# Optimization experiments

Hardware: AMD Instinct MI355X
Metric: run time of the kernel (lower is better)

The kernel has to match this reference:

```python
import jax, jax.numpy as jnp
import numpy as np

D_MODEL = 1024
NUM_HEADS = 16
HEAD_DIM = D_MODEL // NUM_HEADS
D_FF = 4 * D_MODEL


def setup_inputs() -> dict:
    key = jax.random.key(0)
    ks = jax.random.split(key, 16)
    s = 0.02
    inp = {
        "x": jax.random.normal(ks[0], (2, 2048, D_MODEL), dtype=jnp.float32),
        "w_q": jax.random.normal(ks[1], (D_MODEL, D_MODEL), dtype=jnp.float32) * s,
        "b_q": jnp.zeros((D_MODEL,), jnp.float32),
        "w_k": jax.random.normal(ks[2], (D_MODEL, D_MODEL), dtype=jnp.float32) * s,
        "b_k": jnp.zeros((D_MODEL,), jnp.float32),
        "w_v": jax.random.normal(ks[3], (D_MODEL, D_MODEL), dtype=jnp.float32) * s,
        "b_v": jnp.zeros((D_MODEL,), jnp.float32),
        "w_o": jax.random.normal(ks[4], (D_MODEL, D_MODEL), dtype=jnp.float32) * s,
        "b_o": jnp.zeros((D_MODEL,), jnp.float32),
        "w_ff1": jax.random.normal(ks[5], (D_MODEL, D_FF), dtype=jnp.float32) * s,
        "b_ff1": jnp.zeros((D_FF,), jnp.float32),
        "w_ff2": jax.random.normal(ks[6], (D_FF, D_MODEL), dtype=jnp.float32) * s,
        "b_ff2": jnp.zeros((D_MODEL,), jnp.float32),
        "ln1_g": jnp.ones((D_MODEL,), jnp.float32),
        "ln1_b": jnp.zeros((D_MODEL,), jnp.float32),
        "ln2_g": jnp.ones((D_MODEL,), jnp.float32),
        "ln2_b": jnp.zeros((D_MODEL,), jnp.float32),
    }
    return inp


def layer_norm(x, g, b, eps=1e-5):
    mu = jnp.mean(x, axis=-1, keepdims=True)
    var = jnp.var(x, axis=-1, keepdims=True)
    return (x - mu) * jax.lax.rsqrt(var + eps) * g + b


def encoder_block(x, w_q, b_q, w_k, b_k, w_v, b_v, w_o, b_o,
                  w_ff1, b_ff1, w_ff2, b_ff2, ln1_g, ln1_b, ln2_g, ln2_b):
    B, S, _ = x.shape
    # QKV projections -> [B, H, S, hd]
    def proj(w, b):
        return (x @ w + b).reshape(B, S, NUM_HEADS, HEAD_DIM).transpose(0, 2, 1, 3)
    q, k, v = proj(w_q, b_q), proj(w_k, b_k), proj(w_v, b_v)
    scale = 1.0 / jnp.sqrt(jnp.float32(HEAD_DIM))
    score = jnp.einsum('bhqd,bhkd->bhqk', q, k) * scale  # [B,H,S,S]
    attn = jax.nn.softmax(score, axis=-1)
    ctx = jnp.einsum('bhqk,bhkd->bhqd', attn, v)
    ctx = ctx.transpose(0, 2, 1, 3).reshape(B, S, D_MODEL)
    attn_out = ctx @ w_o + b_o
    # AddNorm1 (dropout = identity at inference)
    h = layer_norm(x + attn_out, ln1_g, ln1_b)
    # FFN
    ff = jax.nn.relu(h @ w_ff1 + b_ff1) @ w_ff2 + b_ff2
    # AddNorm2
    return layer_norm(h + ff, ln2_g, ln2_b)


def reference(x, w_q, b_q, w_k, b_k, w_v, b_v, w_o, b_o,
              w_ff1, b_ff1, w_ff2, b_ff2, ln1_g, ln1_b, ln2_g, ln2_b):
    return encoder_block(x, w_q, b_q, w_k, b_k, w_v, b_v, w_o, b_o,
                         w_ff1, b_ff1, w_ff2, b_ff2, ln1_g, ln1_b, ln2_g, ln2_b)
```

## Files before the change

kernel.cpp:

```cpp
#include <hip/hip_runtime.h>
#include <hip/hip_bf16.h>

typedef __attribute__((ext_vector_type(8))) short short8;
typedef __attribute__((ext_vector_type(4))) float f32x4;
typedef unsigned short u16;

constexpr float CSC = 0.18033688f;

__device__ __forceinline__ u16 f2bf(float f) {
    __hip_bfloat16 h = __float2bfloat16(f);
    return __builtin_bit_cast(u16, h);
}
__device__ __forceinline__ float bf2f(u16 u) {
    __hip_bfloat16 h = __builtin_bit_cast(__hip_bfloat16, u);
    return __bfloat162float(h);
}

#define GLD16(g, l) __builtin_amdgcn_global_load_lds( \
    (const __attribute__((address_space(1))) void*)(g), \
    (__attribute__((address_space(3))) void*)(l), 16, 0, 0)

__global__ __launch_bounds__(256) void cast_bf16_kernel(
    const float* __restrict__ src, u16* __restrict__ dst, int n4)
{
    int i = blockIdx.x * 256 + threadIdx.x;
    if (i >= n4) return;
    float4 v = ((const float4*)src)[i];
    *(ushort4*)(dst + 4 * (size_t)i) =
        make_ushort4(f2bf(v.x), f2bf(v.y), f2bf(v.z), f2bf(v.w));
}

__global__ __launch_bounds__(256) void transpose_cast_kernel(
    const float* __restrict__ src, u16* __restrict__ dst, int R, int C)
{
    __shared__ float tile[32][33];
    const int bx = blockIdx.x * 32, by = blockIdx.y * 32;
    const int tx = threadIdx.x & 31, ty = threadIdx.x >> 5;
    #pragma unroll
    for (int i = 0; i < 32; i += 8)
        tile[ty + i][tx] = src[(size_t)(by + ty + i) * C + bx + tx];
    __syncthreads();
    #pragma unroll
    for (int i = 0; i < 32; i += 8)
        dst[(size_t)(bx + ty + i) * R + by + tx] = f2bf(tile[tx][ty + i]);
}

__global__ __launch_bounds__(256) void concat_bias_kernel(
    const float* __restrict__ a, const float* __restrict__ b,
    const float* __restrict__ c, float* __restrict__ d)
{
    int i = blockIdx.x * 256 + threadIdx.x;
    if (i < 1024) { d[i] = a[i]; d[1024 + i] = b[i]; d[2048 + i] = c[i]; }
}

template<bool RELU, int TM, bool QKV>
__global__ __launch_bounds__(256, 2) void gemm_bt(
    const u16* __restrict__ A, const u16* __restrict__ BT,
    const float* __restrict__ bias, u16* __restrict__ C,
    u16* __restrict__ VT, int M, int N, int K)
{
    __shared__ __align__(16) u16 As[TM * 32];
    __shared__ __align__(16) u16 Bs[128 * 32];
    constexpr int MW = TM / 32;
    constexpr int NCH_A = TM * 4;
    constexpr int NITER = (NCH_A + 512) / 256;
    const int t = threadIdx.x;
    const int wave = t >> 6, lane = t & 63;
    const int quad = lane >> 4, l16 = lane & 15;
    const int wm = (wave >> 1) * (TM / 2), wn = (wave & 1) * 64;
    const size_t rowA = (size_t)blockIdx.x * TM;
    const size_t rowB = (size_t)blockIdx.y * 128;

    f32x4 acc[MW][4] = {};

    for (int k0 = 0; k0 < K; k0 += 32) {
        __syncthreads();
        #pragma unroll
        for (int j = 0; j < NITER; ++j) {
            const int cb = j * 256 + wave * 64;
            const int c = cb + lane;
            if (j * 256 < NCH_A) {
                const int m = c >> 2, kq = c & 3;
                GLD16(A + (rowA + m) * K + k0 + kq * 8, As + cb * 8);
            } else {
                const int c2 = c - NCH_A;
                const int m = c2 >> 2, kq = c2 & 3;
                GLD16(BT + (rowB + m) * K + k0 + kq * 8, Bs + (cb - NCH_A) * 8);
            }
        }
        __syncthreads();
        short8 af[MW], bf[4];
        #pragma unroll
        for (int i = 0; i < MW; ++i)
            af[i] = *(const short8*)(As + (wm + i * 16 + l16) * 32 + quad * 8);
        #pragma unroll
        for (int j = 0; j < 4; ++j)
            bf[j] = *(const short8*)(Bs + (wn + j * 16 + l16) * 32 + quad * 8);
        #pragma unroll
        for (int i = 0; i < MW; ++i)
            #pragma unroll
            for (int j = 0; j < 4; ++j)
                acc[i][j] = __builtin_amdgcn_mfma_f32_16x16x32_bf16(
                    af[i], bf[j], acc[i][j], 0, 0, 0);
    }

    if (QKV && (int)blockIdx.y >= 16) {
        #pragma unroll
        for (int i = 0; i < MW; ++i) {
            #pragma unroll
            for (int j = 0; j < 4; ++j) {
                const int vcol = (int)rowB + wn + j * 16 + l16 - 2048;
                const int hh = vcol >> 6, dd = vcol & 63;
                const float bv = bias[vcol + 2048];
                const int row0 = (int)rowA + wm + i * 16 + quad * 4;
                const int bb = row0 >> 11, ss = row0 & 2047;
                ushort4 pk;
                pk.x = f2bf(acc[i][j][0] + bv);
                pk.y = f2bf(acc[i][j][1] + bv);
                pk.z = f2bf(acc[i][j][2] + bv);
                pk.w = f2bf(acc[i][j][3] + bv);
                *(ushort4*)(VT + ((size_t)(bb * 16 + hh) * 64 + dd) * 2048 + ss) = pk;
            }
        }
    } else {
        const float sc = (QKV && (int)blockIdx.y < 8) ? CSC : 1.0f;
        #pragma unroll
        for (int i = 0; i < MW; ++i) {
            #pragma unroll
            for (int j = 0; j < 4; ++j) {
                const int col = (int)rowB + wn + j * 16 + l16;
                const float bv = bias[col];
                #pragma unroll
                for (int r = 0; r < 4; ++r) {
                    const int row = (int)rowA + wm + i * 16 + quad * 4 + r;
                    float v = (acc[i][j][r] + bv) * sc;
                    if (RELU) v = fmaxf(v, 0.f);
                    C[(size_t)row * N + col] = f2bf(v);
                }
            }
        }
    }
}

__global__ __launch_bounds__(256, 3) void flash_attn(
    const u16* __restrict__ qkv, const u16* __restrict__ vt,
    u16* __restrict__ ctx)
{
    __shared__ __align__(16) u16 Ks[64 * 64];
    __shared__ __align__(16) u16 Vs[64 * 64];
    __shared__ __align__(16) u16 Ps[4][32 * 72];
    const int t = threadIdx.x;
    const int wave = t >> 6, lane = t & 63;
    const int quad = lane >> 4, l16 = lane & 15;
    const int h = blockIdx.y, b = blockIdx.z;
    const int q0 = blockIdx.x * 128 + wave * 32;
    const size_t rowbase = (size_t)b * 2048;
    const u16* kb = qkv + rowbase * 3072 + 1024 + h * 64;
    const u16* vb = vt + (size_t)(b * 16 + h) * 64 * 2048;
    u16* pw = Ps[wave];

    short8 aq[2][2];
    #pragma unroll
    for (int mt = 0; mt < 2; ++mt)
        #pragma unroll
        for (int ks = 0; ks < 2; ++ks)
            aq[mt][ks] = *(const short8*)(qkv +
                (rowbase + q0 + mt * 16 + l16) * 3072 + h * 64 + ks * 32 + quad * 8);

    f32x4 o[2][4] = {};
    float lp[2][4] = {};

    for (int kv0 = 0; kv0 < 2048; kv0 += 64) {
        __syncthreads();
        #pragma unroll
        for (int j = 0; j < 2; ++j) {
            const int cb = j * 256 + wave * 64;
            const int slot = cb + lane;
            const int row = slot >> 3;
            const int kq = (slot & 7) ^ (row & 7);
            GLD16(kb + (size_t)(kv0 + row) * 3072 + kq * 8, Ks + cb * 8);
            GLD16(vb + (size_t)row * 2048 + kv0 + kq * 8, Vs + cb * 8);
        }
        __syncthreads();

        f32x4 s[2][4] = {};
        #pragma unroll
        for (int ks = 0; ks < 2; ++ks) {
            short8 bk[4];
            #pragma unroll
            for (int nt = 0; nt < 4; ++nt)
                bk[nt] = *(const short8*)(Ks +
                    ((nt * 16 + l16) * 8 + ((ks * 4 + quad) ^ (l16 & 7))) * 8);
            #pragma unroll
            for (int mt = 0; mt < 2; ++mt)
                #pragma unroll
                for (int nt = 0; nt < 4; ++nt)
                    s[mt][nt] = __builtin_amdgcn_mfma_f32_16x16x32_bf16(
                        aq[mt][ks], bk[nt], s[mt][nt], 0, 0, 0);
        }

        #pragma unroll
        for (int mt = 0; mt < 2; ++mt) {
            #pragma unroll
            for (int r = 0; r < 4; ++r) {
                const float p0 = exp2f(s[mt][0][r]);
                const float p1 = exp2f(s[mt][1][r]);
                const float p2 = exp2f(s[mt][2][r]);
                const float p3 = exp2f(s[mt][3][r]);
                lp[mt][r] += (p0 + p1) + (p2 + p3);
                u16* pp = pw + (mt * 16 + quad * 4 + r) * 72 + l16;
                pp[0] = f2bf(p0); pp[16] = f2bf(p1);
                pp[32] = f2bf(p2); pp[48] = f2bf(p3);
            }
        }

        #pragma unroll
        for (int ks = 0; ks < 2; ++ks) {
            short8 bv[4];
            #pragma unroll
            for (int dt = 0; dt < 4; ++dt)
                bv[dt] = *(const short8*)(Vs +
                    ((dt * 16 + l16) * 8 + ((ks * 4 + quad) ^ (l16 & 7))) * 8);
            #pragma unroll
            for (int mt = 0; mt < 2; ++mt) {
                const short8 ap = *(const short8*)(pw +
                    (mt * 16 + l16) * 72 + ks * 32 + quad * 8);
                #pragma unroll
                for (int dt = 0; dt < 4; ++dt)
                    o[mt][dt] = __builtin_amdgcn_mfma_f32_16x16x32_bf16(
                        ap, bv[dt], o[mt][dt], 0, 0, 0);
            }
        }
    }

    #pragma unroll
    for (int mt = 0; mt < 2; ++mt) {
        #pragma unroll
        for (int r = 0; r < 4; ++r) {
            float rs = lp[mt][r];
            #pragma unroll
            for (int msk = 1; msk < 16; msk <<= 1)
                rs += __shfl_xor(rs, msk, 64);
            const float inv = 1.0f / rs;
            const size_t row = rowbase + q0 + mt * 16 + quad * 4 + r;
            #pragma unroll
            for (int dt = 0; dt < 4; ++dt)
                ctx[row * 1024 + h * 64 + dt * 16 + l16] =
                    f2bf(o[mt][dt][r] * inv);
        }
    }
}

__global__ __launch_bounds__(256) void add_norm_kernel(
    const float* __restrict__ a, const u16* __restrict__ res,
    const float* __restrict__ g, const float* __restrict__ bb,
    float* __restrict__ out32, u16* __restrict__ out16)
{
    __shared__ float red[8];
    const int row = blockIdx.x, t = threadIdx.x;
    const int wave = t >> 6, lane = t & 63;
    const size_t base = (size_t)row * 1024 + t * 4;
    float4 av = *(const float4*)(a + base);
    float v0 = av.x + bf2f(res[base]);
    float v1 = av.y + bf2f(res[base + 1]);
    float v2 = av.z + bf2f(res[base + 2]);
    float v3 = av.w + bf2f(res[base + 3]);
    float sum = v0 + v1 + v2 + v3;
    float sq  = v0 * v0 + v1 * v1 + v2 * v2 + v3 * v3;
    #pragma unroll
    for (int msk = 1; msk < 64; msk <<= 1) {
        sum += __shfl_xor(sum, msk, 64);
        sq  += __shfl_xor(sq,  msk, 64);
    }
    if (lane == 0) { red[wave] = sum; red[wave + 4] = sq; }
    __syncthreads();
    sum = red[0] + red[1] + red[2] + red[3];
    sq  = red[4] + red[5] + red[6] + red[7];
    const float mu  = sum * (1.f / 1024.f);
    const float var = sq * (1.f / 1024.f) - mu * mu;
    const float rstd = rsqrtf(var + 1e-5f);
    const int c = t * 4;
    float o0 = (v0 - mu) * rstd * g[c + 0] + bb[c + 0];
    float o1 = (v1 - mu) * rstd * g[c + 1] + bb[c + 1];
    float o2 = (v2 - mu) * rstd * g[c + 2] + bb[c + 2];
    float o3 = (v3 - mu) * rstd * g[c + 3] + bb[c + 3];
    *(float4*)(out32 + base) = make_float4(o0, o1, o2, o3);
    if (out16)
        *(ushort4*)(out16 + base) = make_ushort4(f2bf(o0), f2bf(o1), f2bf(o2), f2bf(o3));
}

extern "C" void kernel_launch(void* const* d_in, const int* in_sizes, int n_in,
                              void* d_out, int out_size, void* d_ws, size_t ws_size,
                              hipStream_t stream)
{
    const float* x     = (const float*)d_in[0];
    const float* w_q   = (const float*)d_in[1];
    const float* b_q   = (const float*)d_in[2];
    const float* w_k   = (const float*)d_in[3];
    const float* b_k   = (const float*)d_in[4];
    const float* w_v   = (const float*)d_in[5];
    const float* b_v   = (const float*)d_in[6];
    const float* w_o   = (const float*)d_in[7];
    const float* b_o   = (const float*)d_in[8];
    const float* w_ff1 = (const float*)d_in[9];
    const float* b_ff1 = (const float*)d_in[10];
    const float* w_ff2 = (const float*)d_in[11];
    const float* b_ff2 = (const float*)d_in[12];
    const float* ln1_g = (const float*)d_in[13];
    const float* ln1_b = (const float*)d_in[14];
    const float* ln2_g = (const float*)d_in[15];
    const float* ln2_b = (const float*)d_in[16];

    char* ws = (char*)d_ws;
    u16*   xb    = (u16*)(ws);
    u16*   wqkvT = (u16*)(ws + (8ull  << 20));
    u16*   woT   = (u16*)(ws + (14ull << 20));
    u16*   wf1T  = (u16*)(ws + (16ull << 20));
    u16*   wf2T  = (u16*)(ws + (24ull << 20));
    float* bqkv  = (float*)(ws + (32ull << 20));
    u16*   qkv   = (u16*)(ws + (33ull << 20));
    u16*   ctx   = (u16*)(ws + (57ull << 20));
    u16*   ao    = (u16*)(ws + (65ull << 20));
    float* h32   = (float*)(ws + (73ull << 20));
    u16*   hb    = (u16*)(ws + (89ull << 20));
    u16*   ff    = (u16*)(ws + (97ull << 20));
    u16*   vt    = (u16*)(ws + (97ull << 20));
    u16*   y     = (u16*)(ws + (129ull << 20));

    cast_bf16_kernel<<<4096, 256, 0, stream>>>(x, xb, 1024 * 1024);
    transpose_cast_kernel<<<dim3(32, 32),  256, 0, stream>>>(w_q,   wqkvT,                1024, 1024);
    transpose_cast_kernel<<<dim3(32, 32),  256, 0, stream>>>(w_k,   wqkvT + 1024 * 1024,  1024, 1024);
    transpose_cast_kernel<<<dim3(32, 32),  256, 0, stream>>>(w_v,   wqkvT + 2048 * 1024,  1024, 1024);
    transpose_cast_kernel<<<dim3(32, 32),  256, 0, stream>>>(w_o,   woT,                  1024, 1024);
    transpose_cast_kernel<<<dim3(128, 32), 256, 0, stream>>>(w_ff1, wf1T,                 1024, 4096);
    transpose_cast_kernel<<<dim3(32, 128), 256, 0, stream>>>(w_ff2, wf2T,                 4096, 1024);
    concat_bias_kernel<<<4, 256, 0, stream>>>(b_q, b_k, b_v, bqkv);

    gemm_bt<false, 128, true ><<<dim3(32, 24), 256, 0, stream>>>(xb, wqkvT, bqkv, qkv, vt, 4096, 3072, 1024);
    flash_attn<<<dim3(16, 16, 2), 256, 0, stream>>>(qkv, vt, ctx);
    gemm_bt<false, 64, false><<<dim3(64, 8), 256, 0, stream>>>(ctx, woT, b_o, ao, nullptr, 4096, 1024, 1024);
    add_norm_kernel<<<4096, 256, 0, stream>>>(x, ao, ln1_g, ln1_b, h32, hb);
    gemm_bt<true, 128, false><<<dim3(32, 32), 256, 0, stream>>>(hb, wf1T, b_ff1, ff, nullptr, 4096, 4096, 1024);
    gemm_bt<false, 64, false><<<dim3(64, 8),  256, 0, stream>>>(ff, wf2T, b_ff2, y,  nullptr, 4096, 1024, 4096);
    add_norm_kernel<<<4096, 256, 0, stream>>>(h32, y, ln2_g, ln2_b, (float*)d_out, nullptr);
}
```

Measured before the change: 401.4 us.

## Split-K output GEMMs with fused residual norm, smaller attention tiles, merged weight prep

```diff
diff --git a/kernel.cpp b/kernel.cpp
--- a/kernel.cpp
+++ b/kernel.cpp
@@ -4,16 +4,13 @@
 typedef __attribute__((ext_vector_type(8))) short short8;
 typedef __attribute__((ext_vector_type(4))) float f32x4;
 typedef unsigned short u16;
+typedef unsigned int u32;
 
 constexpr float CSC = 0.18033688f;
 
 __device__ __forceinline__ u16 f2bf(float f) {
     __hip_bfloat16 h = __float2bfloat16(f);
     return __builtin_bit_cast(u16, h);
-}
-__device__ __forceinline__ float bf2f(u16 u) {
-    __hip_bfloat16 h = __builtin_bit_cast(__hip_bfloat16, u);
-    return __bfloat162float(h);
 }
 
 #define GLD16(g, l) __builtin_amdgcn_global_load_lds( \
@@ -45,12 +42,33 @@
         dst[(size_t)(bx + ty + i) * R + by + tx] = f2bf(tile[tx][ty + i]);
 }
 
-__global__ __launch_bounds__(256) void concat_bias_kernel(
-    const float* __restrict__ a, const float* __restrict__ b,
-    const float* __restrict__ c, float* __restrict__ d)
-{
-    int i = blockIdx.x * 256 + threadIdx.x;
-    if (i < 1024) { d[i] = a[i]; d[1024 + i] = b[i]; d[2048 + i] = c[i]; }
+__global__ __launch_bounds__(256) void transpose4_bias_kernel(
+    const float* __restrict__ w0, const float* __restrict__ w1,
+    const float* __restrict__ w2, const float* __restrict__ w3,
+    u16* __restrict__ dqkv, u16* __restrict__ d3,
+    const float* __restrict__ bq, const float* __restrict__ bk,
+    const float* __restrict__ bv, float* __restrict__ bout)
+{
+    const int z = blockIdx.z;
+    if (z == 4) {
+        if (blockIdx.y != 0 || blockIdx.x >= 3) return;
+        const float* src = blockIdx.x == 0 ? bq : (blockIdx.x == 1 ? bk : bv);
+        for (int i = threadIdx.x; i < 1024; i += 256)
+            bout[blockIdx.x * 1024 + i] = src[i];
+        return;
+    }
+    const float* src = z == 0 ? w0 : (z == 1 ? w1 : (z == 2 ? w2 : w3));
+    u16* dst = z < 3 ? dqkv + (size_t)z * 1024 * 1024 : d3;
+    __shared__ float tile[32][33];
+    const int bx = blockIdx.x * 32, by = blockIdx.y * 32;
+    const int tx = threadIdx.x & 31, ty = threadIdx.x >> 5;
+    #pragma unroll
+    for (int i = 0; i < 32; i += 8)
+        tile[ty + i][tx] = src[(size_t)(by + ty + i) * 1024 + bx + tx];
+    __syncthreads();
+    #pragma unroll
+    for (int i = 0; i < 32; i += 8)
+        dst[(size_t)(bx + ty + i) * 1024 + by + tx] = f2bf(tile[tx][ty + i]);
 }
 
 template<bool RELU, int TM, bool QKV>
@@ -142,33 +160,97 @@
     }
 }
 
-__global__ __launch_bounds__(256, 3) void flash_attn(
+template<int TM>
+__global__ __launch_bounds__(256, 2) void gemm_bt_sk(
+    const u16* __restrict__ A, const u16* __restrict__ BT,
+    float* __restrict__ Cp0, float* __restrict__ Cp1,
+    int M, int N, int K, int Kspl)
+{
+    __shared__ __align__(16) u16 As[TM * 32];
+    __shared__ __align__(16) u16 Bs[128 * 32];
+    constexpr int MW = TM / 32;
+    constexpr int NCH_A = TM * 4;
+    constexpr int NITER = (NCH_A + 512) / 256;
+    const int t = threadIdx.x;
+    const int wave = t >> 6, lane = t & 63;
+    const int quad = lane >> 4, l16 = lane & 15;
+    const int wm = (wave >> 1) * (TM / 2), wn = (wave & 1) * 64;
+    const size_t rowA = (size_t)blockIdx.x * TM;
+    const size_t rowB = (size_t)blockIdx.y * 128;
+    const int kbeg = blockIdx.z * Kspl;
+
+    f32x4 acc[MW][4] = {};
+
+    for (int k0 = kbeg; k0 < kbeg + Kspl; k0 += 32) {
+        __syncthreads();
+        #pragma unroll
+        for (int j = 0; j < NITER; ++j) {
+            const int cb = j * 256 + wave * 64;
+            const int c = cb + lane;
+            if (j * 256 < NCH_A) {
+                const int m = c >> 2, kq = c & 3;
+                GLD16(A + (rowA + m) * K + k0 + kq * 8, As + cb * 8);
+            } else {
+                const int c2 = c - NCH_A;
+                const int m = c2 >> 2, kq = c2 & 3;
+                GLD16(BT + (rowB + m) * K + k0 + kq * 8, Bs + (cb - NCH_A) * 8);
+            }
+        }
+        __syncthreads();
+        short8 af[MW], bf[4];
+        #pragma unroll
+        for (int i = 0; i < MW; ++i)
+            af[i] = *(const short8*)(As + (wm + i * 16 + l16) * 32 + quad * 8);
+        #pragma unroll
+        for (int j = 0; j < 4; ++j)
+            bf[j] = *(const short8*)(Bs + (wn + j * 16 + l16) * 32 + quad * 8);
+        #pragma unroll
+        for (int i = 0; i < MW; ++i)
+            #pragma unroll
+            for (int j = 0; j < 4; ++j)
+                acc[i][j] = __builtin_amdgcn_mfma_f32_16x16x32_bf16(
+                    af[i], bf[j], acc[i][j], 0, 0, 0);
+    }
+
+    float* out = blockIdx.z == 0 ? Cp0 : Cp1;
+    #pragma unroll
+    for (int i = 0; i < MW; ++i)
+        #pragma unroll
+        for (int j = 0; j < 4; ++j) {
+            const int col = (int)rowB + wn + j * 16 + l16;
+            #pragma unroll
+            for (int r = 0; r < 4; ++r) {
+                const int row = (int)rowA + wm + i * 16 + quad * 4 + r;
+                out[(size_t)row * N + col] = acc[i][j][r];
+            }
+        }
+}
+
+__global__ __launch_bounds__(256, 4) void flash_attn(
     const u16* __restrict__ qkv, const u16* __restrict__ vt,
     u16* __restrict__ ctx)
 {
     __shared__ __align__(16) u16 Ks[64 * 64];
     __shared__ __align__(16) u16 Vs[64 * 64];
-    __shared__ __align__(16) u16 Ps[4][32 * 72];
+    __shared__ __align__(16) u16 Ps[4 * 16 * 72];
     const int t = threadIdx.x;
     const int wave = t >> 6, lane = t & 63;
     const int quad = lane >> 4, l16 = lane & 15;
     const int h = blockIdx.y, b = blockIdx.z;
-    const int q0 = blockIdx.x * 128 + wave * 32;
+    const int q0 = blockIdx.x * 64 + wave * 16;
     const size_t rowbase = (size_t)b * 2048;
     const u16* kb = qkv + rowbase * 3072 + 1024 + h * 64;
     const u16* vb = vt + (size_t)(b * 16 + h) * 64 * 2048;
-    u16* pw = Ps[wave];
-
-    short8 aq[2][2];
-    #pragma unroll
-    for (int mt = 0; mt < 2; ++mt)
-        #pragma unroll
-        for (int ks = 0; ks < 2; ++ks)
-            aq[mt][ks] = *(const short8*)(qkv +
-                (rowbase + q0 + mt * 16 + l16) * 3072 + h * 64 + ks * 32 + quad * 8);
-
-    f32x4 o[2][4] = {};
-    float lp[2][4] = {};
+    u16* pw = Ps + wave * 16 * 72;
+
+    short8 aq[2];
+    #pragma unroll
+    for (int ksb = 0; ksb < 2; ++ksb)
+        aq[ksb] = *(const short8*)(qkv +
+            (rowbase + q0 + l16) * 3072 + h * 64 + ksb * 32 + quad * 8);
+
+    f32x4 o[4] = {};
+    float lp = 0.f;
 
     for (int kv0 = 0; kv0 < 2048; kv0 += 64) {
         __syncthreads();
@@ -183,88 +265,75 @@
         }
         __syncthreads();
 
-        f32x4 s[2][4] = {};
-        #pragma unroll
-        for (int ks = 0; ks < 2; ++ks) {
-            short8 bk[4];
-            #pragma unroll
-            for (int nt = 0; nt < 4; ++nt)
-                bk[nt] = *(const short8*)(Ks +
-                    ((nt * 16 + l16) * 8 + ((ks * 4 + quad) ^ (l16 & 7))) * 8);
-            #pragma unroll
-            for (int mt = 0; mt < 2; ++mt)
-                #pragma unroll
-                for (int nt = 0; nt < 4; ++nt)
-                    s[mt][nt] = __builtin_amdgcn_mfma_f32_16x16x32_bf16(
-                        aq[mt][ks], bk[nt], s[mt][nt], 0, 0, 0);
-        }
-
-        #pragma unroll
-        for (int mt = 0; mt < 2; ++mt) {
-            #pragma unroll
-            for (int r = 0; r < 4; ++r) {
-                const float p0 = exp2f(s[mt][0][r]);
-                const float p1 = exp2f(s[mt][1][r]);
-                const float p2 = exp2f(s[mt][2][r]);
-                const float p3 = exp2f(s[mt][3][r]);
-                lp[mt][r] += (p0 + p1) + (p2 + p3);
-                u16* pp = pw + (mt * 16 + quad * 4 + r) * 72 + l16;
-                pp[0] = f2bf(p0); pp[16] = f2bf(p1);
-                pp[32] = f2bf(p2); pp[48] = f2bf(p3);
-            }
-        }
-
-        #pragma unroll
-        for (int ks = 0; ks < 2; ++ks) {
-            short8 bv[4];
-            #pragma unroll
-            for (int dt = 0; dt < 4; ++dt)
-                bv[dt] = *(const short8*)(Vs +
-                    ((dt * 16 + l16) * 8 + ((ks * 4 + quad) ^ (l16 & 7))) * 8);
-            #pragma unroll
-            for (int mt = 0; mt < 2; ++mt) {
-                const short8 ap = *(const short8*)(pw +
-                    (mt * 16 + l16) * 72 + ks * 32 + quad * 8);
-                #pragma unroll
-                for (int dt = 0; dt < 4; ++dt)
-                    o[mt][dt] = __builtin_amdgcn_mfma_f32_16x16x32_bf16(
-                        ap, bv[dt], o[mt][dt], 0, 0, 0);
-            }
-        }
-    }
-
-    #pragma unroll
-    for (int mt = 0; mt < 2; ++mt) {
-        #pragma unroll
-        for (int r = 0; r < 4; ++r) {
-            float rs = lp[mt][r];
-            #pragma unroll
-            for (int msk = 1; msk < 16; msk <<= 1)
-                rs += __shfl_xor(rs, msk, 64);
-            const float inv = 1.0f / rs;
-            const size_t row = rowbase + q0 + mt * 16 + quad * 4 + r;
-            #pragma unroll
-            for (int dt = 0; dt < 4; ++dt)
-                ctx[row * 1024 + h * 64 + dt * 16 + l16] =
-                    f2bf(o[mt][dt][r] * inv);
-        }
-    }
-}
-
-__global__ __launch_bounds__(256) void add_norm_kernel(
-    const float* __restrict__ a, const u16* __restrict__ res,
-    const float* __restrict__ g, const float* __restrict__ bb,
+        f32x4 st[4] = {};
+        #pragma unroll
+        for (int ksb = 0; ksb < 2; ++ksb) {
+            #pragma unroll
+            for (int mt = 0; mt < 4; ++mt) {
+                const short8 ak = *(const short8*)(Ks +
+                    ((mt * 16 + l16) * 8 + ((ksb * 4 + quad) ^ (l16 & 7))) * 8);
+                st[mt] = __builtin_amdgcn_mfma_f32_16x16x32_bf16(
+                    ak, aq[ksb], st[mt], 0, 0, 0);
+            }
+        }
+
+        #pragma unroll
+        for (int mt = 0; mt < 4; ++mt) {
+            const float p0 = exp2f(st[mt][0]);
+            const float p1 = exp2f(st[mt][1]);
+            const float p2 = exp2f(st[mt][2]);
+            const float p3 = exp2f(st[mt][3]);
+            lp += (p0 + p1) + (p2 + p3);
+            const u32 d0 = (u32)f2bf(p0) | ((u32)f2bf(p1) << 16);
+            const u32 d1 = (u32)f2bf(p2) | ((u32)f2bf(p3) << 16);
+            *(uint2*)(pw + l16 * 72 + mt * 16 + quad * 4) = make_uint2(d0, d1);
+        }
+
+        #pragma unroll
+        for (int ksb = 0; ksb < 2; ++ksb) {
+            const short8 ap = *(const short8*)(pw + l16 * 72 + ksb * 32 + quad * 8);
+            #pragma unroll
+            for (int dt = 0; dt < 4; ++dt) {
+                const short8 bv = *(const short8*)(Vs +
+                    ((dt * 16 + l16) * 8 + ((ksb * 4 + quad) ^ (l16 & 7))) * 8);
+                o[dt] = __builtin_amdgcn_mfma_f32_16x16x32_bf16(
+                    ap, bv, o[dt], 0, 0, 0);
+            }
+        }
+    }
+
+    lp += __shfl_xor(lp, 16, 64);
+    lp += __shfl_xor(lp, 32, 64);
+
+    #pragma unroll
+    for (int r = 0; r < 4; ++r) {
+        const float inv = 1.0f / __shfl(lp, quad * 4 + r, 64);
+        const size_t row = rowbase + q0 + quad * 4 + r;
+        #pragma unroll
+        for (int dt = 0; dt < 4; ++dt)
+            ctx[row * 1024 + h * 64 + dt * 16 + l16] = f2bf(o[dt][r] * inv);
+    }
+}
+
+__global__ __launch_bounds__(256) void add_norm_p_kernel(
+    const float* __restrict__ a, const float* __restrict__ p0,
+    const float* __restrict__ p1, const float* __restrict__ cb,
+    const float* __restrict__ g, const float* __restrict__ bbv,
     float* __restrict__ out32, u16* __restrict__ out16)
 {
     __shared__ float red[8];
     const int row = blockIdx.x, t = threadIdx.x;
     const int wave = t >> 6, lane = t & 63;
     const size_t base = (size_t)row * 1024 + t * 4;
+    const int c = t * 4;
     float4 av = *(const float4*)(a + base);
-    float v0 = av.x + bf2f(res[base]);
-    float v1 = av.y + bf2f(res[base + 1]);
-    float v2 = av.z + bf2f(res[base + 2]);
-    float v3 = av.w + bf2f(res[base + 3]);
+    float4 q0 = *(const float4*)(p0 + base);
+    float4 q1 = *(const float4*)(p1 + base);
+    float4 cv = *(const float4*)(cb + c);
+    float v0 = av.x + q0.x + q1.x + cv.x;
+    float v1 = av.y + q0.y + q1.y + cv.y;
+    float v2 = av.z + q0.z + q1.z + cv.z;
+    float v3 = av.w + q0.w + q1.w + cv.w;
     float sum = v0 + v1 + v2 + v3;
     float sq  = v0 * v0 + v1 * v1 + v2 * v2 + v3 * v3;
     #pragma unroll
@@ -279,11 +348,10 @@
     const float mu  = sum * (1.f / 1024.f);
     const float var = sq * (1.f / 1024.f) - mu * mu;
     const float rstd = rsqrtf(var + 1e-5f);
-    const int c = t * 4;
-    float o0 = (v0 - mu) * rstd * g[c + 0] + bb[c + 0];
-    float o1 = (v1 - mu) * rstd * g[c + 1] + bb[c + 1];
-    float o2 = (v2 - mu) * rstd * g[c + 2] + bb[c + 2];
-    float o3 = (v3 - mu) * rstd * g[c + 3] + bb[c + 3];
+    float o0 = (v0 - mu) * rstd * g[c + 0] + bbv[c + 0];
+    float o1 = (v1 - mu) * rstd * g[c + 1] + bbv[c + 1];
+    float o2 = (v2 - mu) * rstd * g[c + 2] + bbv[c + 2];
+    float o3 = (v3 - mu) * rstd * g[c + 3] + bbv[c + 3];
     *(float4*)(out32 + base) = make_float4(o0, o1, o2, o3);
     if (out16)
         *(ushort4*)(out16 + base) = make_ushort4(f2bf(o0), f2bf(o1), f2bf(o2), f2bf(o3));
@@ -320,27 +388,32 @@
     float* bqkv  = (float*)(ws + (32ull << 20));
     u16*   qkv   = (u16*)(ws + (33ull << 20));
     u16*   ctx   = (u16*)(ws + (57ull << 20));
-    u16*   ao    = (u16*)(ws + (65ull << 20));
-    float* h32   = (float*)(ws + (73ull << 20));
-    u16*   hb    = (u16*)(ws + (89ull << 20));
-    u16*   ff    = (u16*)(ws + (97ull << 20));
-    u16*   vt    = (u16*)(ws + (97ull << 20));
-    u16*   y     = (u16*)(ws + (129ull << 20));
+    float* h32   = (float*)(ws + (65ull << 20));
+    u16*   hb    = (u16*)(ws + (81ull << 20));
+    u16*   ff    = (u16*)(ws + (89ull << 20));
+    u16*   vt    = (u16*)(ws + (121ull << 20));
+    float* pO0   = (float*)(ws + (33ull << 20));
+    float* pO1   = (float*)(ws + (121ull << 20));
+    float* pF0   = (float*)(ws + (33ull << 20));
+    float* pF1   = (float*)(ws + (49ull << 20));
 
     cast_bf16_kernel<<<4096, 256, 0, stream>>>(x, xb, 1024 * 1024);
-    transpose_cast_kernel<<<dim3(32, 32),  256, 0, stream>>>(w_q,   wqkvT,                1024, 1024);
-    transpose_cast_kernel<<<dim3(32, 32),  256, 0, stream>>>(w_k,   wqkvT + 1024 * 1024,  1024, 1024);
-    transpose_cast_kernel<<<dim3(32, 32),  256, 0, stream>>>(w_v,   wqkvT + 2048 * 1024,  1024, 1024);
-    transpose_cast_kernel<<<dim3(32, 32),  256, 0, stream>>>(w_o,   woT,                  1024, 1024);
-    transpose_cast_kernel<<<dim3(128, 32), 256, 0, stream>>>(w_ff1, wf1T,                 1024, 4096);
-    transpose_cast_kernel<<<dim3(32, 128), 256, 0, stream>>>(w_ff2, wf2T,                 4096, 1024);
-    concat_bias_kernel<<<4, 256, 0, stream>>>(b_q, b_k, b_v, bqkv);
-
-    gemm_bt<false, 128, true ><<<dim3(32, 24), 256, 0, stream>>>(xb, wqkvT, bqkv, qkv, vt, 4096, 3072, 1024);
-    flash_attn<<<dim3(16, 16, 2), 256, 0, stream>>>(qkv, vt, ctx);
-    gemm_bt<false, 64, false><<<dim3(64, 8), 256, 0, stream>>>(ctx, woT, b_o, ao, nullptr, 4096, 1024, 1024);
-    add_norm_kernel<<<4096, 256, 0, stream>>>(x, ao, ln1_g, ln1_b, h32, hb);
-    gemm_bt<true, 128, false><<<dim3(32, 32), 256, 0, stream>>>(hb, wf1T, b_ff1, ff, nullptr, 4096, 4096, 1024);
-    gemm_bt<false, 64, false><<<dim3(64, 8),  256, 0, stream>>>(ff, wf2T, b_ff2, y,  nullptr, 4096, 1024, 4096);
-    add_norm_kernel<<<4096, 256, 0, stream>>>(h32, y, ln2_g, ln2_b, (float*)d_out, nullptr);
-}
+    transpose4_bias_kernel<<<dim3(32, 32, 5), 256, 0, stream>>>(
+        w_q, w_k, w_v, w_o, wqkvT, woT, b_q, b_k, b_v, bqkv);
+    transpose_cast_kernel<<<dim3(128, 32), 256, 0, stream>>>(w_ff1, wf1T, 1024, 4096);
+    transpose_cast_kernel<<<dim3(32, 128), 256, 0, stream>>>(w_ff2, wf2T, 4096, 1024);
+
+    gemm_bt<false, 128, true ><<<dim3(32, 24), 256, 0, stream>>>(
+        xb, wqkvT, bqkv, qkv, vt, 4096, 3072, 1024);
+    flash_attn<<<dim3(32, 16, 2), 256, 0, stream>>>(qkv, vt, ctx);
+    gemm_bt_sk<128><<<dim3(32, 8, 2), 256, 0, stream>>>(
+        ctx, woT, pO0, pO1, 4096, 1024, 1024, 512);
+    add_norm_p_kernel<<<4096, 256, 0, stream>>>(
+        x, pO0, pO1, b_o, ln1_g, ln1_b, h32, hb);
+    gemm_bt<true, 128, false><<<dim3(32, 32), 256, 0, stream>>>(
+        hb, wf1T, b_ff1, ff, nullptr, 4096, 4096, 1024);
+    gemm_bt_sk<128><<<dim3(32, 8, 2), 256, 0, stream>>>(
+        ff, wf2T, pF0, pF1, 4096, 1024, 4096, 2048);
+    add_norm_p_kernel<<<4096, 256, 0, stream>>>(
+        h32, pF0, pF1, b_ff2, ln2_g, ln2_b, (float*)d_out, nullptr);
+}
```

Result: faster. 371.9 us (-7.3%).
